# Performance work log

Hardware: AMD Instinct MI355X
Metric: run time of the kernel (lower is better)

The kernel has to match this reference:

```python
import jax, jax.numpy as jnp
import numpy as np

DEGREE = 8


def _askey_wilson_basis(x, a, b, c, d, q, degree):
    # Iterative 3-term recurrence (same math as the recursive torch version).
    # x: (batch, input_dim); a,b,c,d,q: scalars broadcast over x.
    basis = [jnp.ones_like(x)]
    if degree >= 1:
        p1 = (2 * (1 + a * b * q) * x - (a + b) * (1 + c * d * q)) / (1 + a * b * c * d * q ** 2)
        basis.append(p1)
    for n in range(2, degree + 1):
        An = (1 - a * b * q ** (n - 1)) * (1 - c * d * q ** (n - 1)) * (1 - a * b * c * d * q ** (2 * n - 2))
        An = An / ((1 - a * b * c * d * q ** (2 * n - 1)) * (1 - a * b * c * d * q ** (2 * n)))
        Cn = (1 - q ** n) * (1 - a * b * q ** (n - 1)) * (1 - c * d * q ** (n - 1)) * (1 - a * b * c * d * q ** (2 * n - 2))
        Cn = Cn / ((1 - a * b * c * d * q ** (2 * n - 2)) * (1 - a * b * c * d * q ** (2 * n - 1)))
        pn = ((2 * x - An) * basis[n - 1] - Cn * basis[n - 2]) / (1 - q ** n)
        basis.append(pn)
    return jnp.stack(basis, axis=-1)  # (batch, input_dim, degree+1)


def setup_inputs() -> dict:
    key = jax.random.key(0)
    k1, k2, k3, k4, k5, k6, k7 = jax.random.split(key, 7)
    input_dim, output_dim, degree = 1024, 1024, DEGREE
    batch = 8192
    x = jax.random.normal(k1, (batch, input_dim), dtype=jnp.float32)
    a = jax.random.normal(k2, (1,), dtype=jnp.float32)
    b = jax.random.normal(k3, (1,), dtype=jnp.float32)
    c = jax.random.normal(k4, (1,), dtype=jnp.float32)
    d = jax.random.normal(k5, (1,), dtype=jnp.float32)
    q = jax.random.normal(k6, (1,), dtype=jnp.float32)
    std = 1.0 / (input_dim * (degree + 1))
    coeffs = jax.random.normal(k7, (input_dim, output_dim, degree + 1), dtype=jnp.float32) * std
    return {"x": x, "a": a, "b": b, "c": c, "d": d, "q": q, "coeffs": coeffs}


def reference(x, a, b, c, d, q, coeffs) -> jnp.ndarray:
    a0, b0, c0, d0, q0 = a[0], b[0], c[0], d[0], q[0]
    basis = _askey_wilson_basis(x, a0, b0, c0, d0, q0, DEGREE)  # (b, i, d+1)
    y = jnp.einsum('bid,iod->bo', basis, coeffs)
    return y
```

## Files before the change

### kernel.cpp

```cpp
#include <hip/hip_runtime.h>
#include <cstdint>

typedef unsigned short u16;
typedef __bf16 bf16x8 __attribute__((ext_vector_type(8)));
typedef float f32x4 __attribute__((ext_vector_type(4)));

#define M_DIM 8192
#define N_DIM 1024
#define I_DIM 1024
#define NDEG 8
#define K_DIM (I_DIM * NDEG)
#define BM 256
#define BN 128
#define BK 64
#define NT (K_DIM / BK)
#define A_TILE (BM * BK)
#define B_TILE (BN * BK)

__device__ __forceinline__ u16 f2bf(float f) {
    union { float f; uint32_t u; } v; v.f = f;
    return (u16)((v.u + 0x7FFFu + ((v.u >> 16) & 1u)) >> 16);
}

__device__ __forceinline__ void gload_lds16(const u16* g, u16* l) {
    auto lp = reinterpret_cast<__attribute__((address_space(3))) uint32_t*>(
        reinterpret_cast<uintptr_t>(l));
    __builtin_amdgcn_global_load_lds(reinterpret_cast<const uint32_t*>(g), lp, 16, 0, 0);
}

__global__ __launch_bounds__(256) void aw_transform(
    const float* __restrict__ coeffs, u16* __restrict__ Bt, float* __restrict__ bias)
{
    __shared__ float lds[32][292];
    int bi = blockIdx.x >> 5, bo = blockIdx.x & 31;
    int i0 = bi * 32, o0 = bo * 32;
    int t = threadIdx.x;

    {
        int r = t >> 3, s = t & 7;
        const float4* src = (const float4*)(coeffs + ((size_t)(i0 + r) * N_DIM + o0) * 9);
#pragma unroll
        for (int j = 0; j < 9; ++j) {
            float4 v = src[s * 9 + j];
            *(float4*)&lds[r][(s * 9 + j) * 4] = v;
        }
    }
    __syncthreads();

    {
        int c = t >> 3, s2 = t & 7;
        u16 ob[32];
#pragma unroll
        for (int rr = 0; rr < 4; ++rr)
#pragma unroll
            for (int dd = 0; dd < 8; ++dd)
                ob[rr * 8 + dd] = f2bf(lds[s2 * 4 + rr][c * 9 + 1 + dd]);
        uint4* dst = (uint4*)(Bt + (size_t)(o0 + c) * K_DIM + (size_t)i0 * 8 + s2 * 32);
        const uint4* sp = (const uint4*)ob;
#pragma unroll
        for (int u = 0; u < 4; ++u) dst[u] = sp[u];
    }

    if (t < 32) {
        float sum = 0.f;
#pragma unroll
        for (int rr = 0; rr < 32; ++rr) sum += lds[rr][t * 9];
        atomicAdd(&bias[o0 + t], sum);
    }
}

__global__ void aw_basis(const float* __restrict__ x,
                         const float* __restrict__ pa, const float* __restrict__ pb,
                         const float* __restrict__ pc, const float* __restrict__ pd,
                         const float* __restrict__ pq,
                         u16* __restrict__ A, int row0)
{
    int t  = blockIdx.x * 256 + threadIdx.x;
    int rb = t >> 7;
    int g  = t & 127;
    int i0 = g << 3;
    int b  = row0 + rb;

    float a = *pa, bb = *pb, c = *pc, d = *pd, q = *pq;
    float ab = a * bb, cd = c * d, abcd = ab * cd;

    float qp[17];
    qp[0] = 1.f;
#pragma unroll
    for (int k = 1; k <= 16; ++k) qp[k] = qp[k - 1] * q;

    float den1 = 1.f + abcd * q * q;
    float c1x = 2.f * (1.f + ab * q) / den1;
    float c1c = -(a + bb) * (1.f + cd * q) / den1;

    float An[9], Cn[9], Sn[9];
#pragma unroll
    for (int n = 2; n <= 8; ++n) {
        float t1 = 1.f - ab * qp[n - 1];
        float t2 = 1.f - cd * qp[n - 1];
        float t3 = 1.f - abcd * qp[2 * n - 2];
        float t4 = 1.f - abcd * qp[2 * n - 1];
        float t5 = 1.f - abcd * qp[2 * n];
        An[n] = (t1 * t2 * t3) / (t4 * t5);
        Cn[n] = ((1.f - qp[n]) * t1 * t2 * t3) / (t3 * t4);
        Sn[n] = 1.f / (1.f - qp[n]);
    }

    const float4* x4 = (const float4*)(x + (size_t)b * I_DIM + i0);
    float4 v0 = x4[0], v1 = x4[1];
    float xv[8] = {v0.x, v0.y, v0.z, v0.w, v1.x, v1.y, v1.z, v1.w};

    u16 ob[64];
#pragma unroll
    for (int j = 0; j < 8; ++j) {
        float xj = xv[j];
        float p1 = c1x * xj + c1c;
        ob[j * 8 + 0] = f2bf(p1);
        float pm2 = 1.f, pm1 = p1;
#pragma unroll
        for (int n = 2; n <= 8; ++n) {
            float pn = ((2.f * xj - An[n]) * pm1 - Cn[n] * pm2) * Sn[n];
            ob[j * 8 + n - 1] = f2bf(pn);
            pm2 = pm1; pm1 = pn;
        }
    }

    uint4* dst = (uint4*)(A + (size_t)rb * K_DIM + (size_t)i0 * 8);
    const uint4* s = (const uint4*)ob;
#pragma unroll
    for (int u = 0; u < 8; ++u) dst[u] = s[u];
}

__global__ __launch_bounds__(512) void aw_gemm(
    const u16* __restrict__ A,
    const u16* __restrict__ B,
    const float* __restrict__ bias,
    float* __restrict__ C,
    int row0, int rowBlocks)
{
    __shared__ alignas(16) u16 smem[3 * A_TILE + 3 * B_TILE];
    u16* As = smem;
    u16* Bs = smem + 3 * A_TILE;

    int nwg = rowBlocks * 8;
    int bid = blockIdx.x;
    int per = nwg >> 3;
    int logical = (bid & 7) * per + (bid >> 3);
    int rowBlk = logical >> 3;
    int colBlk = logical & 7;

    const int tid  = threadIdx.x;
    const int lane = tid & 63;
    const int wid  = tid >> 6;
    const int quad = wid & 3;
    const int wr   = quad >> 1;
    const int wc   = quad & 1;
    const int myKs = wid >> 2;

    const u16* gA[4]; const u16* gB[2];
    int ldsA[4], ldsB[2];
#pragma unroll
    for (int j = 0; j < 4; ++j) {
        int idx = j * 512 + tid;
        int r = idx >> 3, sl = idx & 7;
        gA[j] = A + (size_t)rowBlk * BM * K_DIM + (size_t)r * K_DIM + ((sl ^ (r & 7)) << 3);
        ldsA[j] = idx << 3;
    }
#pragma unroll
    for (int j = 0; j < 2; ++j) {
        int idx = j * 512 + tid;
        int r = idx >> 3, sl = idx & 7;
        gB[j] = B + (size_t)colBlk * BN * K_DIM + (size_t)r * K_DIM + ((sl ^ (r & 7)) << 3);
        ldsB[j] = idx << 3;
    }

    int offA[8], offB[4];
#pragma unroll
    for (int mi = 0; mi < 8; ++mi) {
        int r = wr * 128 + mi * 16 + (lane & 15);
        int s = myKs * 4 + (lane >> 4);
        offA[mi] = r * 128 + ((s ^ (r & 7)) << 4);
    }
#pragma unroll
    for (int ni = 0; ni < 4; ++ni) {
        int r = wc * 64 + ni * 16 + (lane & 15);
        int s = myKs * 4 + (lane >> 4);
        offB[ni] = r * 128 + ((s ^ (r & 7)) << 4);
    }

    f32x4 acc[8][4];
#pragma unroll
    for (int mi = 0; mi < 8; ++mi)
#pragma unroll
        for (int ni = 0; ni < 4; ++ni)
            acc[mi][ni] = (f32x4){0.f, 0.f, 0.f, 0.f};

    auto stage = [&](int kt, int buf) {
        const int k0 = kt * BK;
        u16* dA = As + buf * A_TILE;
        u16* dB = Bs + buf * B_TILE;
        gload_lds16(gA[0] + k0, dA + ldsA[0]);
        gload_lds16(gA[1] + k0, dA + ldsA[1]);
        gload_lds16(gA[2] + k0, dA + ldsA[2]);
        gload_lds16(gA[3] + k0, dA + ldsA[3]);
        gload_lds16(gB[0] + k0, dB + ldsB[0]);
        gload_lds16(gB[1] + k0, dB + ldsB[1]);
    };

    stage(0, 0);
    stage(1, 1);
    asm volatile("s_waitcnt vmcnt(6)" ::: "memory");
    __builtin_amdgcn_s_barrier();

    int buf = 0;
    for (int t = 0; t < NT; ++t) {
        const char* aB = (const char*)(As + buf * A_TILE);
        const char* bB = (const char*)(Bs + buf * B_TILE);
        int nb = buf + 2; if (nb >= 3) nb -= 3;
        const bool pf = (t + 2 < NT);

        bf16x8 fa[8], fb[4];
#pragma unroll
        for (int mi = 0; mi < 8; ++mi) fa[mi] = *(const bf16x8*)(aB + offA[mi]);
#pragma unroll
        for (int ni = 0; ni < 4; ++ni) fb[ni] = *(const bf16x8*)(bB + offB[ni]);

        if (pf) stage(t + 2, nb);
        __builtin_amdgcn_s_barrier();

        __builtin_amdgcn_s_setprio(1);
#pragma unroll
        for (int mi = 0; mi < 8; ++mi)
#pragma unroll
            for (int ni = 0; ni < 4; ++ni)
                acc[mi][ni] = __builtin_amdgcn_mfma_f32_16x16x32_bf16(
                    fa[mi], fb[ni], acc[mi][ni], 0, 0, 0);
        __builtin_amdgcn_s_setprio(0);

        if (pf)               { asm volatile("s_waitcnt vmcnt(6)" ::: "memory"); }
        else if (t + 1 < NT)  { asm volatile("s_waitcnt vmcnt(0)" ::: "memory"); }
        __builtin_amdgcn_s_barrier();

        buf += 1; if (buf >= 3) buf -= 3;
    }

    float* red = (float*)smem;
    if (myKs == 1) {
        f32x4* dst = (f32x4*)red + quad * 2048;
#pragma unroll
        for (int mi = 0; mi < 8; ++mi)
#pragma unroll
            for (int ni = 0; ni < 4; ++ni)
                dst[(mi * 4 + ni) * 64 + lane] = acc[mi][ni];
    }
    __syncthreads();
    if (myKs == 0) {
        const f32x4* src = (const f32x4*)red + quad * 2048;
#pragma unroll
        for (int mi = 0; mi < 8; ++mi)
#pragma unroll
            for (int ni = 0; ni < 4; ++ni) {
                f32x4 p = src[(mi * 4 + ni) * 64 + lane];
                acc[mi][ni] += p;
            }

        int gRow = row0 + rowBlk * BM + wr * 128;
        int gCol = colBlk * BN + wc * 64;
#pragma unroll
        for (int mi = 0; mi < 8; ++mi) {
#pragma unroll
            for (int ni = 0; ni < 4; ++ni) {
                int rr = gRow + mi * 16 + ((lane >> 4) << 2);
                int cc = gCol + ni * 16 + (lane & 15);
                float bv = bias[cc];
                float* dst = C + (size_t)rr * N_DIM + cc;
#pragma unroll
                for (int j = 0; j < 4; ++j) dst[(size_t)j * N_DIM] = acc[mi][ni][j] + bv;
            }
        }
    }
}

extern "C" void kernel_launch(void* const* d_in, const int* in_sizes, int n_in,
                              void* d_out, int out_size, void* d_ws, size_t ws_size,
                              hipStream_t stream)
{
    const float* x      = (const float*)d_in[0];
    const float* pa     = (const float*)d_in[1];
    const float* pb     = (const float*)d_in[2];
    const float* pc     = (const float*)d_in[3];
    const float* pd     = (const float*)d_in[4];
    const float* pq     = (const float*)d_in[5];
    const float* coeffs = (const float*)d_in[6];
    float* out = (float*)d_out;

    float* bias = (float*)d_ws;
    const size_t biasBytes = 4096;
    u16* Bt = (u16*)((char*)d_ws + biasBytes);
    const size_t btBytes = (size_t)N_DIM * K_DIM * sizeof(u16);
    u16* Abuf = (u16*)((char*)d_ws + biasBytes + btBytes);
    size_t used = biasBytes + btBytes;
    size_t avail = ws_size > used ? ws_size - used : 0;

    int chunk = M_DIM;
    while (chunk > 256 && (size_t)chunk * K_DIM * sizeof(u16) > avail) chunk >>= 1;

    hipMemsetAsync(bias, 0, N_DIM * sizeof(float), stream);
    aw_transform<<<1024, 256, 0, stream>>>(coeffs, Bt, bias);

    for (int row0 = 0; row0 < M_DIM; row0 += chunk) {
        aw_basis<<<(chunk * 128) / 256, 256, 0, stream>>>(x, pa, pb, pc, pd, pq, Abuf, row0);
        int rowBlocks = chunk / BM;
        aw_gemm<<<rowBlocks * 8, 512, 0, stream>>>(Abuf, Bt, bias, out, row0, rowBlocks);
    }
}
```

Baseline: 192.3 us.

## Deepen GEMM pipeline with register double-buffered fragments and one barrier per step

Restructures the main K loop to prefetch three LDS stages ahead and double-buffer the MFMA operand fragments in registers. The LDS reads for the next tile are issued before the current tile's MFMAs, so they can overlap. Each iteration now needs one workgroup barrier instead of two. It also sets launch bounds to request two workgroups per CU, which caps the register budget while the 128-float accumulator stays live, so register spills are a risk.

```diff
diff --git a/kernel.cpp b/kernel.cpp
--- a/kernel.cpp
+++ b/kernel.cpp
@@ -131,7 +131,7 @@
     for (int u = 0; u < 8; ++u) dst[u] = s[u];
 }
 
-__global__ __launch_bounds__(512) void aw_gemm(
+__global__ __launch_bounds__(512, 2) void aw_gemm(
     const u16* __restrict__ A,
     const u16* __restrict__ B,
     const float* __restrict__ bias,
@@ -206,28 +206,15 @@
         gload_lds16(gB[0] + k0, dB + ldsB[0]);
         gload_lds16(gB[1] + k0, dB + ldsB[1]);
     };
-
-    stage(0, 0);
-    stage(1, 1);
-    asm volatile("s_waitcnt vmcnt(6)" ::: "memory");
-    __builtin_amdgcn_s_barrier();
-
-    int buf = 0;
-    for (int t = 0; t < NT; ++t) {
+    auto rdfrags = [&](bf16x8 (&fa)[8], bf16x8 (&fb)[4], int buf) {
         const char* aB = (const char*)(As + buf * A_TILE);
         const char* bB = (const char*)(Bs + buf * B_TILE);
-        int nb = buf + 2; if (nb >= 3) nb -= 3;
-        const bool pf = (t + 2 < NT);
-
-        bf16x8 fa[8], fb[4];
 #pragma unroll
         for (int mi = 0; mi < 8; ++mi) fa[mi] = *(const bf16x8*)(aB + offA[mi]);
 #pragma unroll
         for (int ni = 0; ni < 4; ++ni) fb[ni] = *(const bf16x8*)(bB + offB[ni]);
-
-        if (pf) stage(t + 2, nb);
-        __builtin_amdgcn_s_barrier();
-
+    };
+    auto domfma = [&](bf16x8 (&fa)[8], bf16x8 (&fb)[4]) {
         __builtin_amdgcn_s_setprio(1);
 #pragma unroll
         for (int mi = 0; mi < 8; ++mi)
@@ -236,13 +223,35 @@
                 acc[mi][ni] = __builtin_amdgcn_mfma_f32_16x16x32_bf16(
                     fa[mi], fb[ni], acc[mi][ni], 0, 0, 0);
         __builtin_amdgcn_s_setprio(0);
-
-        if (pf)               { asm volatile("s_waitcnt vmcnt(6)" ::: "memory"); }
-        else if (t + 1 < NT)  { asm volatile("s_waitcnt vmcnt(0)" ::: "memory"); }
-        __builtin_amdgcn_s_barrier();
-
-        buf += 1; if (buf >= 3) buf -= 3;
-    }
+    };
+
+#define ITER(T, CA, CB, NA, NB)                                               \
+    do {                                                                      \
+        if ((T) + 3 < NT) stage((T) + 3, ((T) + 3) % 3);                      \
+        if ((T) + 1 < NT) rdfrags(NA, NB, ((T) + 1) % 3);                     \
+        domfma(CA, CB);                                                       \
+        asm volatile("s_waitcnt lgkmcnt(0)" ::: "memory");                    \
+        __builtin_amdgcn_sched_barrier(0);                                    \
+        if ((T) + 3 < NT)      { asm volatile("s_waitcnt vmcnt(6)" ::: "memory"); } \
+        else if ((T) + 1 < NT) { asm volatile("s_waitcnt vmcnt(0)" ::: "memory"); } \
+        __builtin_amdgcn_s_barrier();                                         \
+    } while (0)
+
+    stage(0, 0); stage(1, 1); stage(2, 2);
+    asm volatile("s_waitcnt vmcnt(6)" ::: "memory");
+    __builtin_amdgcn_s_barrier();
+
+    bf16x8 pa[8], pb[4], qa[8], qb[4];
+    rdfrags(pa, pb, 0);
+    asm volatile("s_waitcnt lgkmcnt(0)" ::: "memory");
+    __builtin_amdgcn_sched_barrier(0);
+    __builtin_amdgcn_s_barrier();
+
+    for (int t = 0; t < NT; t += 2) {
+        ITER(t,     pa, pb, qa, qb);
+        ITER(t + 1, qa, qb, pa, pb);
+    }
+#undef ITER
 
     float* red = (float*)smem;
     if (myKs == 1) {
```

Result: no change. 193.3 us (+0.5%).
